# Kernel tuning notes

Measured on AMD Instinct MI355X. Metric: run time of the kernel, lower is better.

## Reference

```python
import jax, jax.numpy as jnp
import numpy as np

LORA_SCALE = 1.0 / 4.0  # alpha=1, rank=4
TAU_IOU = 0.1


def lora(x, W, A, B):
    # x @ W.T + (x @ A.T) @ B.T * scaling
    return x @ W.T + (x @ A.T) @ B.T * LORA_SCALE


def decode(h, Wd1, bd1, Wd2, bd2):
    # mask_decoder: Linear(embed,64) -> ReLU -> Linear(64,1)
    return (jax.nn.relu(h @ Wd1.T + bd1) @ Wd2.T + bd2)[..., 0]


def setup_inputs() -> dict:
    key = jax.random.key(0)
    ks = jax.random.split(key, 16)
    B, N, I, E, R = 2, 8192, 32, 128, 4
    s = lambda k, shape, f=0.05: jax.random.normal(k, shape, dtype=jnp.float32) * f
    return {
        "points": jax.random.normal(ks[0], (B, N, 3), dtype=jnp.float32),
        "pos_coords": jax.random.normal(ks[1], (B, I, 3), dtype=jnp.float32),
        "W1": s(ks[2], (64, 3), 0.3),
        "A1": s(ks[3], (R, 3), 0.3),
        "B1": s(ks[4], (64, R), 0.3),
        "W2": s(ks[5], (E, 64), 0.1),
        "A2": s(ks[6], (R, 64), 0.1),
        "B2": s(ks[7], (E, R), 0.1),
        "Wp": s(ks[8], (E, 3), 0.3),
        "bp": s(ks[9], (E,), 0.1),
        "Wd1": s(ks[10], (64, E), 0.1),
        "bd1": s(ks[11], (64,), 0.1),
        "Wd2": s(ks[12], (1, 64), 0.1),
        "bd2": s(ks[13], (1,), 0.1),
    }


def npc_neg_coords(initial_logits, pos_coords, key):
    # Vectorized replacement of the double python loop: for each (b,i),
    # uniformly sample one j with iou[b,i,j] >= tau (Gumbel-max trick);
    # if none, leave zeros.
    B, I, N = initial_logits.shape
    masks = (jax.nn.sigmoid(initial_logits) > 0.5).astype(initial_logits.dtype)  # [B,I,N]
    inter = jnp.einsum("bin,bjn->bij", masks, masks)
    m_sum = masks.sum(axis=2)  # [B,I]
    union = m_sum[:, :, None] + m_sum[:, None, :] - inter
    iou = inter / (union + 1e-6)
    iou = iou * (1.0 - jnp.eye(I, dtype=iou.dtype))  # zero diagonal
    cand = iou >= TAU_IOU  # [B,I,I]
    gumbel = -jnp.log(-jnp.log(jax.random.uniform(key, cand.shape, minval=1e-20, maxval=1.0)))
    scores = jnp.where(cand, gumbel, -jnp.inf)
    idx = jnp.argmax(scores, axis=-1)  # [B,I]
    valid = cand.any(axis=-1)  # [B,I]
    picked = jnp.take_along_axis(pos_coords, idx[..., None], axis=1)  # [B,I,3]
    return jnp.where(valid[..., None], picked, 0.0)


def reference(points, pos_coords, W1, A1, B1, W2, A2, B2, Wp, bp, Wd1, bd1, Wd2, bd2):
    # encoder: LoRA(3->64) -> ReLU -> LoRA(64->128)
    point_feats = lora(jax.nn.relu(lora(points, W1, A1, B1)), W2, A2, B2)  # [B,N,E]
    pos_embed = pos_coords @ Wp.T + bp  # [B,I,E]
    # [B,I,N,E] combined features
    initial_logits = decode(point_feats[:, None, :, :] + pos_embed[:, :, None, :], Wd1, bd1, Wd2, bd2)  # [B,I,N]
    neg_coords = npc_neg_coords(initial_logits, pos_coords, jax.random.key(42))
    neg_embed = neg_coords @ Wp.T + bp  # [B,I,E]
    refined_logits = decode(
        point_feats[:, None, :, :] + (pos_embed - neg_embed)[:, :, None, :], Wd1, bd1, Wd2, bd2
    )  # [B,I,N]
    return refined_logits, point_feats
```

## Files before the change

kernel.cpp:

```cpp
#include <hip/hip_runtime.h>

#define B_  2
#define N_  8192
#define I_  32
#define E_  128
#define H_  64
#define BN_ (B_*N_)
#define NW_ (N_/64)

typedef unsigned long long u64;

__device__ float g_pe  [B_*I_*E_];
__device__ float g_v1  [B_*I_*H_];
__device__ float g_v2  [B_*I_*H_];
__device__ float g_wd1t[E_*H_];
__device__ float g_delta[B_*I_*E_];
__device__ float g_u   [H_*BN_];
__device__ u64   g_masks[B_*I_*NW_];
__device__ int   g_inter[B_*I_*I_];

__device__ __forceinline__ unsigned rotl_(unsigned x, unsigned n){ return (x<<n)|(x>>(32u-n)); }

__device__ void threefry_42(unsigned x0, unsigned x1, unsigned* r0, unsigned* r1){
  const unsigned ks0 = 0u, ks1 = 42u, ks2 = 0x1BD11BDAu ^ 0u ^ 42u;
  x0 += ks0; x1 += ks1;
  x0+=x1; x1=rotl_(x1,13); x1^=x0;
  x0+=x1; x1=rotl_(x1,15); x1^=x0;
  x0+=x1; x1=rotl_(x1,26); x1^=x0;
  x0+=x1; x1=rotl_(x1, 6); x1^=x0;
  x0+=ks1; x1+=ks2+1u;
  x0+=x1; x1=rotl_(x1,17); x1^=x0;
  x0+=x1; x1=rotl_(x1,29); x1^=x0;
  x0+=x1; x1=rotl_(x1,16); x1^=x0;
  x0+=x1; x1=rotl_(x1,24); x1^=x0;
  x0+=ks2; x1+=ks0+2u;
  x0+=x1; x1=rotl_(x1,13); x1^=x0;
  x0+=x1; x1=rotl_(x1,15); x1^=x0;
  x0+=x1; x1=rotl_(x1,26); x1^=x0;
  x0+=x1; x1=rotl_(x1, 6); x1^=x0;
  x0+=ks0; x1+=ks1+3u;
  x0+=x1; x1=rotl_(x1,17); x1^=x0;
  x0+=x1; x1=rotl_(x1,29); x1^=x0;
  x0+=x1; x1=rotl_(x1,16); x1^=x0;
  x0+=x1; x1=rotl_(x1,24); x1^=x0;
  x0+=ks1; x1+=ks2+4u;
  x0+=x1; x1=rotl_(x1,13); x1^=x0;
  x0+=x1; x1=rotl_(x1,15); x1^=x0;
  x0+=x1; x1=rotl_(x1,26); x1^=x0;
  x0+=x1; x1=rotl_(x1, 6); x1^=x0;
  x0+=ks2; x1+=ks0+5u;
  *r0 = x0; *r1 = x1;
}

__device__ float jax_uniform_2048(int e){
  unsigned o0, o1;
  threefry_42(0u, (unsigned)e, &o0, &o1);
  unsigned bits = o0 ^ o1;
  float u = __uint_as_float((bits >> 9) | 0x3f800000u) - 1.0f;
  u = u + 1e-20f;
  return fmaxf(1e-20f, u);
}

__global__ void __launch_bounds__(256) prep_kernel(
    const float* __restrict__ pos_coords,
    const float* __restrict__ Wp, const float* __restrict__ bp,
    const float* __restrict__ Wd1,const float* __restrict__ bd1)
{
  __shared__ float t_l [E_*65];
  __shared__ float pe_l[E_];
  const int row = blockIdx.x;
  const int tid = threadIdx.x;

  for (int idx = tid; idx < H_*E_; idx += 256){
    int k = idx >> 7, e = idx & 127;
    t_l[e*65 + k] = Wd1[idx];
  }
  if (tid < E_){
    const int e = tid;
    float s = pos_coords[row*3+0] * Wp[e*3+0];
    s = fmaf(pos_coords[row*3+1], Wp[e*3+1], s);
    s = fmaf(pos_coords[row*3+2], Wp[e*3+2], s);
    const float pe = s + bp[e];
    g_pe[row*E_ + e] = pe;
    pe_l[e] = pe;
  }
  __syncthreads();

  if (row == 0){
    for (int idx = tid; idx < E_*H_; idx += 256){
      int e = idx >> 6, k = idx & 63;
      g_wd1t[idx] = t_l[e*65 + k];
    }
  }
  if (tid < H_){
    const int k = tid;
    float s = 0.f;
    for (int e = 0; e < 128; ++e)
      s = fmaf(pe_l[e], t_l[e*65 + k], s);
    g_v1[row*H_ + k] = s + bd1[k];
  }
}

__global__ void __launch_bounds__(512) enc_kernel(
    const float* __restrict__ points,
    const float* __restrict__ W1, const float* __restrict__ A1,
    const float* __restrict__ B1, const float* __restrict__ W2,
    const float* __restrict__ A2, const float* __restrict__ B2,
    const float* __restrict__ Wd2,const float* __restrict__ bd2,
    float* __restrict__ out_pf)
{
  __shared__ float pf_l[E_*65];
  __shared__ float u_l [64*65];
  const int tid  = threadIdx.x;
  const int w_u  = __builtin_amdgcn_readfirstlane(tid >> 6);
  const int lane = tid & 63;
  const int p0   = blockIdx.x * 64;
  const int p    = p0 + lane;
  const int b    = blockIdx.x >> 7;

  const float x0 = points[p*3+0];
  const float x1 = points[p*3+1];
  const float x2 = points[p*3+2];

  float a1[4];
  #pragma unroll
  for (int r = 0; r < 4; ++r){
    float s = x0 * A1[r*3+0];
    s = fmaf(x1, A1[r*3+1], s);
    s = fmaf(x2, A1[r*3+2], s);
    a1[r] = s;
  }
  float t1[64];
  #pragma unroll
  for (int k = 0; k < 64; ++k){
    float s = x0 * W1[k*3+0];
    s = fmaf(x1, W1[k*3+1], s);
    s = fmaf(x2, W1[k*3+2], s);
    float l = a1[0] * B1[k*4+0];
    l = fmaf(a1[1], B1[k*4+1], l);
    l = fmaf(a1[2], B1[k*4+2], l);
    l = fmaf(a1[3], B1[k*4+3], l);
    t1[k] = fmaxf(fmaf(0.25f, l, s), 0.0f);
  }
  float a2[4];
  #pragma unroll
  for (int r = 0; r < 4; ++r){
    float s = 0.f;
    #pragma unroll
    for (int j = 0; j < 64; ++j) s = fmaf(t1[j], A2[r*64+j], s);
    a2[r] = s;
  }
  float u_p[64];
  #pragma unroll
  for (int k = 0; k < 64; ++k) u_p[k] = 0.f;

  const int e0 = w_u * 16;
  for (int ei = 0; ei < 16; ++ei){
    const int e = e0 + ei;
    float s1 = 0.f;
    #pragma unroll
    for (int j = 0; j < 64; ++j) s1 = fmaf(t1[j], W2[e*64+j], s1);
    float s2 = a2[0] * B2[e*4+0];
    s2 = fmaf(a2[1], B2[e*4+1], s2);
    s2 = fmaf(a2[2], B2[e*4+2], s2);
    s2 = fmaf(a2[3], B2[e*4+3], s2);
    const float pf = fmaf(0.25f, s2, s1);
    pf_l[e*65 + lane] = pf;
    #pragma unroll
    for (int k = 0; k < 64; ++k) u_p[k] = fmaf(pf, g_wd1t[e*64+k], u_p[k]);
  }

  for (int pass = 0; pass < 8; ++pass){
    if (w_u == pass){
      if (pass == 0){
        #pragma unroll
        for (int k = 0; k < 64; ++k) u_l[lane*65 + k] = u_p[k];
      } else {
        #pragma unroll
        for (int k = 0; k < 64; ++k) u_l[lane*65 + k] += u_p[k];
      }
    }
    __syncthreads();
  }

  for (int idx = tid; idx < 64*E_; idx += 512){
    const int pt = idx >> 7, e = idx & 127;
    out_pf[(size_t)p0 * E_ + idx] = pf_l[e*65 + pt];
  }
  for (int idx = tid; idx < 64*64; idx += 512){
    const int k = idx >> 6, pl = idx & 63;
    g_u[(size_t)k * BN_ + p0 + pl] = u_l[pl*65 + k];
  }

  const float bd2v = bd2[0];
  float acc[4];
  #pragma unroll
  for (int ii = 0; ii < 4; ++ii) acc[ii] = 0.f;
  const int ibase = w_u * 4;
  const float* v = g_v1 + ((b * I_ + ibase) << 6);
  for (int k = 0; k < 64; ++k){
    const float wd2k = Wd2[k];
    const float uk = u_l[lane*65 + k];
    #pragma unroll
    for (int ii = 0; ii < 4; ++ii)
      acc[ii] = fmaf(wd2k, fmaxf(uk + v[ii*64 + k], 0.0f), acc[ii]);
  }
  #pragma unroll
  for (int ii = 0; ii < 4; ++ii){
    const int i = ibase + ii;
    u64 bal = __ballot(acc[ii] + bd2v > 0.0f);
    if (lane == 0) g_masks[(size_t)(b * I_ + i) * NW_ + (blockIdx.x & 127)] = bal;
  }
}

__global__ void __launch_bounds__(256) inter_kernel()
{
  const int r   = blockIdx.x;
  const int b   = r >> 5;
  const int tid = threadIdx.x;
  const int j   = tid >> 3;
  const int ws  = (tid & 7) * 16;
  const u64* mi = g_masks + (size_t)r * NW_;
  const u64* mj = g_masks + (size_t)(b*32 + j) * NW_;
  int s = 0;
  #pragma unroll
  for (int w = 0; w < 16; ++w)
    s += __popcll(mi[ws + w] & mj[ws + w]);
  s += __shfl_xor(s, 1, 64);
  s += __shfl_xor(s, 2, 64);
  s += __shfl_xor(s, 4, 64);
  if ((tid & 7) == 0) g_inter[r*32 + j] = s;
}

__global__ void __launch_bounds__(256) sample_kernel(
    const float* __restrict__ pos_coords,
    const float* __restrict__ Wp, const float* __restrict__ bp)
{
  __shared__ int   inter_l[2048];
  __shared__ float nc_l[64][3];
  const int tid = threadIdx.x;

  for (int idx = tid; idx < 2048; idx += 256) inter_l[idx] = g_inter[idx];
  __syncthreads();

  if (tid < 64){
    const int b = tid >> 5;
    const int i = tid & 31;
    const int msum_i = inter_l[(b << 10) + (i << 5) + i];
    float best = -INFINITY; int bestj = 0; bool any = false;
    for (int j = 0; j < 32; ++j){
      const int inter = inter_l[(b << 10) + (i << 5) + j];
      const int msum_j = inter_l[(b << 10) + (j << 5) + j];
      const int uni   = msum_i + msum_j - inter;
      const float iou = (float)inter / ((float)uni + 1e-6f);
      const bool cand = (j != i) && (iou >= 0.1f);
      if (cand){
        any = true;
        const float uu = jax_uniform_2048((tid << 5) + j);
        const float g  = -logf(-logf(uu));
        if (g > best){ best = g; bestj = j; }
      }
    }
    nc_l[tid][0] = any ? pos_coords[(b*32 + bestj)*3 + 0] : 0.f;
    nc_l[tid][1] = any ? pos_coords[(b*32 + bestj)*3 + 1] : 0.f;
    nc_l[tid][2] = any ? pos_coords[(b*32 + bestj)*3 + 2] : 0.f;
  }
  __syncthreads();

  for (int idx = tid; idx < 64*E_; idx += 256){
    const int row = idx >> 7, e = idx & 127;
    float ne = nc_l[row][0] * Wp[e*3+0];
    ne = fmaf(nc_l[row][1], Wp[e*3+1], ne);
    ne = fmaf(nc_l[row][2], Wp[e*3+2], ne);
    ne = ne + bp[e];
    g_delta[idx] = g_pe[idx] - ne;
  }
}

__global__ void __launch_bounds__(256) v2k_kernel(const float* __restrict__ bd1)
{
  const int idx = blockIdx.x * 256 + threadIdx.x;
  const int row = idx >> 6, k = idx & 63;
  float s = 0.f;
  for (int e = 0; e < 128; ++e)
    s = fmaf(g_delta[row*128 + e], g_wd1t[e*64 + k], s);
  g_v2[idx] = s + bd1[k];
}

__global__ void __launch_bounds__(256) dec_kernel(
    const float* __restrict__ Wd2, const float* __restrict__ bd2,
    float* __restrict__ out0)
{
  const int tid  = threadIdx.x;
  const int w_u  = __builtin_amdgcn_readfirstlane(tid >> 6);
  const int lane = tid & 63;
  const int bc   = blockIdx.x;
  const int b    = bc >> 8;
  const int nb   = (bc & 127) << 6;
  const int ih   = (bc >> 7) & 1;
  const int n    = nb + lane;
  const int p    = b * N_ + n;

  float u[64];
  #pragma unroll
  for (int k = 0; k < 64; ++k) u[k] = g_u[(size_t)k * BN_ + p];

  const float bd2v = bd2[0];
  float acc[4];
  #pragma unroll
  for (int ii = 0; ii < 4; ++ii) acc[ii] = 0.f;
  const int ibase = ih * 16 + w_u * 4;
  const float* v = g_v2 + ((b * I_ + ibase) << 6);
  for (int k = 0; k < 64; ++k){
    const float wd2k = Wd2[k];
    const float uk = u[k];
    #pragma unroll
    for (int ii = 0; ii < 4; ++ii)
      acc[ii] = fmaf(wd2k, fmaxf(uk + v[ii*64 + k], 0.0f), acc[ii]);
  }
  #pragma unroll
  for (int ii = 0; ii < 4; ++ii){
    const int i = ibase + ii;
    out0[(size_t)(b * I_ + i) * N_ + n] = acc[ii] + bd2v;
  }
}

extern "C" void kernel_launch(void* const* d_in, const int* in_sizes, int n_in,
                              void* d_out, int out_size, void* d_ws, size_t ws_size,
                              hipStream_t stream)
{
  (void)in_sizes; (void)n_in; (void)out_size; (void)d_ws; (void)ws_size;
  const float* points     = (const float*)d_in[0];
  const float* pos_coords = (const float*)d_in[1];
  const float* W1  = (const float*)d_in[2];
  const float* A1  = (const float*)d_in[3];
  const float* B1  = (const float*)d_in[4];
  const float* W2  = (const float*)d_in[5];
  const float* A2  = (const float*)d_in[6];
  const float* B2  = (const float*)d_in[7];
  const float* Wp  = (const float*)d_in[8];
  const float* bp  = (const float*)d_in[9];
  const float* Wd1 = (const float*)d_in[10];
  const float* bd1 = (const float*)d_in[11];
  const float* Wd2 = (const float*)d_in[12];
  const float* bd2 = (const float*)d_in[13];

  float* out0   = (float*)d_out;
  float* out_pf = out0 + (size_t)B_ * I_ * N_;

  prep_kernel<<<64, 256, 0, stream>>>(pos_coords, Wp, bp, Wd1, bd1);
  enc_kernel<<<256, 512, 0, stream>>>(points, W1, A1, B1, W2, A2, B2,
                                      Wd2, bd2, out_pf);
  inter_kernel<<<64, 256, 0, stream>>>();
  sample_kernel<<<1, 256, 0, stream>>>(pos_coords, Wp, bp);
  v2k_kernel<<<16, 256, 0, stream>>>(bd1);
  dec_kernel<<<512, 256, 0, stream>>>(Wd2, bd2, out0);
}
```

Baseline: 149.6 us.

## Restructure encoder u-projection by output slice and fuse sampling with v2 projection

In the encoder kernel, each wavefront used to accumulate a 64-wide partial u vector over its 16 embedding channels, then the partials were reduced serially across 8 passes with barriers. Now the point features are first written to shared memory, and each wavefront computes 8 u outputs over all 128 channels, writing g_u directly. Separately, the sample and v2k kernels are merged into one 16-block kernel, which removes a launch and the g_delta global round trip. The price is that each sample block recomputes its four rows, and the encoder reads pf_l from shared memory 128 times per lane.

Measured after the change: 149.8 us. About the same (+0.1%).

```diff
diff --git a/kernel.cpp b/kernel.cpp
--- a/kernel.cpp
+++ b/kernel.cpp
@@ -14,7 +14,6 @@
 __device__ float g_v1  [B_*I_*H_];
 __device__ float g_v2  [B_*I_*H_];
 __device__ float g_wd1t[E_*H_];
-__device__ float g_delta[B_*I_*E_];
 __device__ float g_u   [H_*BN_];
 __device__ u64   g_masks[B_*I_*NW_];
 __device__ int   g_inter[B_*I_*I_];
@@ -150,9 +149,6 @@
     for (int j = 0; j < 64; ++j) s = fmaf(t1[j], A2[r*64+j], s);
     a2[r] = s;
   }
-  float u_p[64];
-  #pragma unroll
-  for (int k = 0; k < 64; ++k) u_p[k] = 0.f;
 
   const int e0 = w_u * 16;
   for (int ei = 0; ei < 16; ++ei){
@@ -164,32 +160,30 @@
     s2 = fmaf(a2[1], B2[e*4+1], s2);
     s2 = fmaf(a2[2], B2[e*4+2], s2);
     s2 = fmaf(a2[3], B2[e*4+3], s2);
-    const float pf = fmaf(0.25f, s2, s1);
-    pf_l[e*65 + lane] = pf;
-    #pragma unroll
-    for (int k = 0; k < 64; ++k) u_p[k] = fmaf(pf, g_wd1t[e*64+k], u_p[k]);
-  }
-
-  for (int pass = 0; pass < 8; ++pass){
-    if (w_u == pass){
-      if (pass == 0){
-        #pragma unroll
-        for (int k = 0; k < 64; ++k) u_l[lane*65 + k] = u_p[k];
-      } else {
-        #pragma unroll
-        for (int k = 0; k < 64; ++k) u_l[lane*65 + k] += u_p[k];
-      }
-    }
-    __syncthreads();
-  }
+    pf_l[e*65 + lane] = fmaf(0.25f, s2, s1);
+  }
+  __syncthreads();
+
+  const int kbase = w_u * 8;
+  float uacc[8];
+  #pragma unroll
+  for (int kk = 0; kk < 8; ++kk) uacc[kk] = 0.f;
+  for (int e = 0; e < 128; ++e){
+    const float pf = pf_l[e*65 + lane];
+    #pragma unroll
+    for (int kk = 0; kk < 8; ++kk)
+      uacc[kk] = fmaf(pf, g_wd1t[e*64 + kbase + kk], uacc[kk]);
+  }
+  #pragma unroll
+  for (int kk = 0; kk < 8; ++kk){
+    g_u[(size_t)(kbase + kk) * BN_ + p] = uacc[kk];
+    u_l[lane*65 + kbase + kk] = uacc[kk];
+  }
+  __syncthreads();
 
   for (int idx = tid; idx < 64*E_; idx += 512){
     const int pt = idx >> 7, e = idx & 127;
     out_pf[(size_t)p0 * E_ + idx] = pf_l[e*65 + pt];
-  }
-  for (int idx = tid; idx < 64*64; idx += 512){
-    const int k = idx >> 6, pl = idx & 63;
-    g_u[(size_t)k * BN_ + p0 + pl] = u_l[pl*65 + k];
   }
 
   const float bd2v = bd2[0];
@@ -234,18 +228,22 @@
 
 __global__ void __launch_bounds__(256) sample_kernel(
     const float* __restrict__ pos_coords,
-    const float* __restrict__ Wp, const float* __restrict__ bp)
+    const float* __restrict__ Wp, const float* __restrict__ bp,
+    const float* __restrict__ bd1)
 {
   __shared__ int   inter_l[2048];
-  __shared__ float nc_l[64][3];
-  const int tid = threadIdx.x;
+  __shared__ float delta_l[4*E_];
+  __shared__ float nc_l[4][3];
+  const int tid  = threadIdx.x;
+  const int row0 = blockIdx.x * 4;
 
   for (int idx = tid; idx < 2048; idx += 256) inter_l[idx] = g_inter[idx];
   __syncthreads();
 
-  if (tid < 64){
-    const int b = tid >> 5;
-    const int i = tid & 31;
+  if (tid < 4){
+    const int row = row0 + tid;
+    const int b = row >> 5;
+    const int i = row & 31;
     const int msum_i = inter_l[(b << 10) + (i << 5) + i];
     float best = -INFINITY; int bestj = 0; bool any = false;
     for (int j = 0; j < 32; ++j){
@@ -256,7 +254,7 @@
       const bool cand = (j != i) && (iou >= 0.1f);
       if (cand){
         any = true;
-        const float uu = jax_uniform_2048((tid << 5) + j);
+        const float uu = jax_uniform_2048((row << 5) + j);
         const float g  = -logf(-logf(uu));
         if (g > best){ best = g; bestj = j; }
       }
@@ -267,24 +265,23 @@
   }
   __syncthreads();
 
-  for (int idx = tid; idx < 64*E_; idx += 256){
-    const int row = idx >> 7, e = idx & 127;
-    float ne = nc_l[row][0] * Wp[e*3+0];
-    ne = fmaf(nc_l[row][1], Wp[e*3+1], ne);
-    ne = fmaf(nc_l[row][2], Wp[e*3+2], ne);
+  for (int idx = tid; idx < 4*E_; idx += 256){
+    const int rl = idx >> 7, e = idx & 127;
+    float ne = nc_l[rl][0] * Wp[e*3+0];
+    ne = fmaf(nc_l[rl][1], Wp[e*3+1], ne);
+    ne = fmaf(nc_l[rl][2], Wp[e*3+2], ne);
     ne = ne + bp[e];
-    g_delta[idx] = g_pe[idx] - ne;
-  }
-}
-
-__global__ void __launch_bounds__(256) v2k_kernel(const float* __restrict__ bd1)
-{
-  const int idx = blockIdx.x * 256 + threadIdx.x;
-  const int row = idx >> 6, k = idx & 63;
-  float s = 0.f;
-  for (int e = 0; e < 128; ++e)
-    s = fmaf(g_delta[row*128 + e], g_wd1t[e*64 + k], s);
-  g_v2[idx] = s + bd1[k];
+    delta_l[idx] = g_pe[(row0 + rl)*E_ + e] - ne;
+  }
+  __syncthreads();
+
+  {
+    const int rl = tid >> 6, k = tid & 63;
+    float s = 0.f;
+    for (int e = 0; e < 128; ++e)
+      s = fmaf(delta_l[rl*E_ + e], g_wd1t[e*64 + k], s);
+    g_v2[(row0 + rl)*H_ + k] = s + bd1[k];
+  }
 }
 
 __global__ void __launch_bounds__(256) dec_kernel(
@@ -352,7 +349,6 @@
   enc_kernel<<<256, 512, 0, stream>>>(points, W1, A1, B1, W2, A2, B2,
                                       Wd2, bd2, out_pf);
   inter_kernel<<<64, 256, 0, stream>>>();
-  sample_kernel<<<1, 256, 0, stream>>>(pos_coords, Wp, bp);
-  v2k_kernel<<<16, 256, 0, stream>>>(bd1);
+  sample_kernel<<<16, 256, 0, stream>>>(pos_coords, Wp, bp, bd1);
   dec_kernel<<<512, 256, 0, stream>>>(Wd2, bd2, out0);
 }
```
